# Performance work log

Measured on AMD Instinct MI355X. Metric: run time of the kernel, lower is better.

The kernel has to match this reference:

```python
import jax, jax.numpy as jnp
import numpy as np

C = 256
C8 = C // 8  # query/key channels
B, T, W, H = 4, 8, 32, 32


def setup_inputs() -> dict:
    key = jax.random.key(0)
    ks = jax.random.split(key, 8)
    s = 0.05
    return {
        "x": jax.random.normal(ks[0], (B, C, T, W, H), dtype=jnp.float32),
        "wq": jax.random.normal(ks[1], (C8, C), dtype=jnp.float32) * s,
        "bq": jax.random.normal(ks[2], (C8,), dtype=jnp.float32) * s,
        "wk": jax.random.normal(ks[3], (C8, C), dtype=jnp.float32) * s,
        "bk": jax.random.normal(ks[4], (C8,), dtype=jnp.float32) * s,
        "wv": jax.random.normal(ks[5], (C, C), dtype=jnp.float32) * s,
        "bv": jax.random.normal(ks[6], (C,), dtype=jnp.float32) * s,
        "gamma": jax.random.normal(ks[7], (1,), dtype=jnp.float32),
    }


def reference(x, wq, bq, wk, bk, wv, bv, gamma):
    b, c, t, w, h = x.shape
    n = w * h
    # Faithful to torch: x.view(-1, c, w, h) is a row-major reinterpretation
    xr = jnp.reshape(x, (-1, c, n))  # (m, C, N), m = B*T
    # 1x1 convs == per-pixel linear projections
    q = jnp.einsum("oc,mcn->mno", wq, xr) + bq            # (m, N, C8)
    k = jnp.einsum("oc,mcn->mon", wk, xr) + bk[:, None]   # (m, C8, N)
    v = jnp.einsum("oc,mcn->mon", wv, xr) + bv[:, None]   # (m, C, N)
    energy = jnp.einsum("mic,mcj->mij", q, k)             # (m, N, N), unscaled
    attention = jax.nn.softmax(energy, axis=-1)
    out = jnp.einsum("mcn,mnj->mcj", v, attention)        # V @ A (as in torch code)
    out = jnp.reshape(out, (b, c, t, w, h))
    return gamma * out + x
```

## Files before the change

kernel.cpp:

```cpp
#include <hip/hip_runtime.h>

#define MB    32
#define CCH   256
#define QCH   32
#define NPIX  1024
#define SLICE (CCH * NPIX)
#define L2E   1.44269504088896340736f
#define SHIFT 32.0f

typedef __bf16          bf16x8 __attribute__((ext_vector_type(8)));
typedef __bf16          bf16x4 __attribute__((ext_vector_type(4)));
typedef float           f32x4  __attribute__((ext_vector_type(4)));
typedef unsigned int    u32x4  __attribute__((ext_vector_type(4)));
typedef unsigned short  u16x4  __attribute__((ext_vector_type(4)));

__device__ __forceinline__ unsigned short f2bf(float f) {
    unsigned int u = __builtin_bit_cast(unsigned int, f);
    u += 0x7FFFu + ((u >> 16) & 1u);
    return (unsigned short)(u >> 16);
}
__device__ __forceinline__ u16x4 cvt4(float a, float b, float c, float d) {
    bf16x4 v = { (__bf16)a, (__bf16)b, (__bf16)c, (__bf16)d };
    return __builtin_bit_cast(u16x4, v);
}
__device__ __forceinline__ float bf2f(unsigned short u) {
    unsigned int v = (unsigned int)u << 16;
    return __builtin_bit_cast(float, v);
}
__device__ __forceinline__ bf16x8 ldfrag(const unsigned short* p) {
    u32x4 u = *(const u32x4*)p;
    return __builtin_bit_cast(bf16x8, u);
}

#define WB_OFF  0u
#define QT_OFF  262144u
#define KT_OFF  2359296u
#define V_OFF   4456448u
#define A2F_OFF 21233664u
#define PU_OFF  21364736u
#define WS_NEED 88473600u

__global__ __launch_bounds__(256) void k_prep_w(
    const float* __restrict__ wq, const float* __restrict__ wk,
    const float* __restrict__ wv, unsigned short* __restrict__ Wb)
{
    int i4 = (blockIdx.x * 256 + threadIdx.x) * 4;
    int o = i4 >> 8, c = i4 & 255;
    const float* src = (o < 32) ? wq + (size_t)o * CCH + c
                     : (o < 64) ? wk + (size_t)(o - 32) * CCH + c
                                : wv + (size_t)(o - 64) * CCH + c;
    float4 v = *(const float4*)src;
    *(u16x4*)(Wb + i4) = cvt4(v.x, v.y, v.z, v.w);
}

__global__ __launch_bounds__(256) void k_proj(
    const float* __restrict__ x, const unsigned short* __restrict__ Wb,
    const float* __restrict__ bq, const float* __restrict__ bk,
    const float* __restrict__ bv,
    unsigned short* __restrict__ Qt, unsigned short* __restrict__ Kt,
    unsigned short* __restrict__ V)
{
    __shared__ unsigned short Xs[64 * 268];

    const int t = threadIdx.x, lane = t & 63, w = t >> 6;
    const int lj = lane & 15, q = lane >> 4;
    const int n0 = blockIdx.x * 64;
    const int mi = blockIdx.y;
    const float* xp = x + (size_t)mi * SLICE;

#pragma unroll
    for (int r = 0; r < 8; ++r) {
        int job = t + r * 256;
        int cp = job >> 4;
        int seg = job & 15;
        float4 va = *(const float4*)(xp + (size_t)(2 * cp) * NPIX + n0 + seg * 4);
        float4 vb = *(const float4*)(xp + (size_t)(2 * cp + 1) * NPIX + n0 + seg * 4);
        u16x4 da = cvt4(va.x, va.y, va.z, va.w);
        u16x4 db = cvt4(vb.x, vb.y, vb.z, vb.w);
#pragma unroll
        for (int e = 0; e < 4; ++e) {
            unsigned pk = (unsigned)da[e] | ((unsigned)db[e] << 16);
            *(unsigned*)&Xs[(seg * 4 + e) * 268 + 2 * cp] = pk;
        }
    }
    __syncthreads();

    f32x4 acc[5][4];
#pragma unroll
    for (int i = 0; i < 5; ++i)
#pragma unroll
        for (int b = 0; b < 4; ++b) acc[i][b] = (f32x4){0.f, 0.f, 0.f, 0.f};

    const unsigned short* wbase = Wb + (size_t)(w * 16 + lj) * CCH + q * 8;
    const unsigned short* xbase = &Xs[lj * 268 + q * 8];

#pragma unroll 2
    for (int kc = 0; kc < CCH; kc += 32) {
        bf16x8 a[5];
#pragma unroll
        for (int i = 0; i < 5; ++i)
            a[i] = ldfrag(wbase + (size_t)i * 64 * CCH + kc);
        bf16x8 xb[4];
#pragma unroll
        for (int b = 0; b < 4; ++b)
            xb[b] = ldfrag(xbase + b * 16 * 268 + kc);
#pragma unroll
        for (int i = 0; i < 5; ++i)
#pragma unroll
            for (int b = 0; b < 4; ++b)
                acc[i][b] = __builtin_amdgcn_mfma_f32_16x16x32_bf16(a[i], xb[b], acc[i][b], 0, 0, 0);
    }

#pragma unroll
    for (int i = 0; i < 5; ++i) {
        const int o16 = (w + 4 * i) * 16;
        const int ob = o16 + 4 * q;
        if (o16 < 32) {
            unsigned short* Qp = Qt + (size_t)mi * NPIX * QCH;
            float b0 = bq[ob], b1 = bq[ob + 1], b2 = bq[ob + 2], b3 = bq[ob + 3];
#pragma unroll
            for (int b = 0; b < 4; ++b) {
                int n = n0 + b * 16 + lj;
                *(u16x4*)(Qp + (size_t)n * QCH + ob) =
                    cvt4((acc[i][b][0] + b0) * L2E, (acc[i][b][1] + b1) * L2E,
                         (acc[i][b][2] + b2) * L2E, (acc[i][b][3] + b3) * L2E);
            }
        } else if (o16 < 64) {
            unsigned short* Kp = Kt + (size_t)mi * NPIX * QCH;
            int o2 = ob - 32;
            float b0 = bk[o2], b1 = bk[o2 + 1], b2 = bk[o2 + 2], b3 = bk[o2 + 3];
#pragma unroll
            for (int b = 0; b < 4; ++b) {
                int n = n0 + b * 16 + lj;
                *(u16x4*)(Kp + (size_t)n * QCH + o2) =
                    cvt4(acc[i][b][0] + b0, acc[i][b][1] + b1,
                         acc[i][b][2] + b2, acc[i][b][3] + b3);
            }
        } else {
            unsigned short* Vw = V + (size_t)mi * SLICE;
            const int c16 = (o16 - 64) >> 4;
            const int n05 = n0 >> 5;
            const int cb = (o16 - 64) + 4 * q;
            float bb[4] = { bv[cb], bv[cb + 1], bv[cb + 2], bv[cb + 3] };
            const int ni = lj & 7;
#pragma unroll
            for (int b = 0; b < 4; ++b) {
                int n5 = n05 + (b >> 1);
                int fl = ((2 * b + (lj >> 3)) & 3) * 16 + 4 * q;
                size_t base = ((size_t)(c16 * 32 + n5) * 64 + fl) * 8 + ni;
#pragma unroll
                for (int r = 0; r < 4; ++r)
                    Vw[base + (size_t)r * 8] = f2bf(acc[i][b][r] + bb[r]);
            }
        }
    }
}

__global__ __launch_bounds__(256) void k_stats(
    const unsigned short* __restrict__ Qt, const unsigned short* __restrict__ Kt,
    float* __restrict__ a2f)
{
    const int t = threadIdx.x, lane = t & 63, w = t >> 6;
    const int lj = lane & 15, q = lane >> 4;
    const int n16 = blockIdx.x * 64 + w * 16;
    const int mi = blockIdx.y;
    const unsigned short* Qp = Qt + (size_t)mi * NPIX * QCH;
    const unsigned short* Kp = Kt + (size_t)mi * NPIX * QCH;

    bf16x8 qa = ldfrag(Qp + (size_t)(n16 + lj) * QCH + q * 8);

    float s[4] = { 0.f, 0.f, 0.f, 0.f };
#pragma unroll 8
    for (int jc = 0; jc < NPIX; jc += 16) {
        bf16x8 kb = ldfrag(Kp + (size_t)(jc + lj) * QCH + q * 8);
        f32x4 z = (f32x4){0.f, 0.f, 0.f, 0.f};
        f32x4 e = __builtin_amdgcn_mfma_f32_16x16x32_bf16(qa, kb, z, 0, 0, 0);
#pragma unroll
        for (int r = 0; r < 4; ++r) s[r] += exp2f(e[r] - SHIFT);
    }
#pragma unroll
    for (int msk = 1; msk <= 8; msk <<= 1)
#pragma unroll
        for (int r = 0; r < 4; ++r) s[r] += __shfl_xor(s[r], msk, 64);
    if (lj == 0) {
        float* apo = a2f + (size_t)mi * NPIX;
#pragma unroll
        for (int r = 0; r < 4; ++r)
            apo[n16 + 4 * q + r] = SHIFT + log2f(s[r]);
    }
}

__global__ __launch_bounds__(256) void k_pu(
    const unsigned short* __restrict__ Qt, const unsigned short* __restrict__ Kt,
    const float* __restrict__ a2f, unsigned short* __restrict__ Pu)
{
    __shared__ unsigned short Ps[4][32][36];

    const int t = threadIdx.x, lane = t & 63, w = t >> 6;
    const int lj = lane & 15, q = lane >> 4;
    const int nb = blockIdx.x >> 1;
    const int jh = blockIdx.x & 1;
    const int nw = nb * 128 + w * 32;
    const int mi = blockIdx.y;
    const unsigned short* Qp = Qt + (size_t)mi * NPIX * QCH;
    const unsigned short* Kp = Kt + (size_t)mi * NPIX * QCH;
    const float* ap = a2f + (size_t)mi * NPIX;
    unsigned short* Pup = Pu + (size_t)mi * NPIX * NPIX;

    bf16x8 qa[2];
    f32x4  a4[2];
#pragma unroll
    for (int h = 0; h < 2; ++h) {
        qa[h] = ldfrag(Qp + (size_t)(nw + h * 16 + lj) * QCH + q * 8);
        a4[h] = *(const f32x4*)(ap + nw + h * 16 + 4 * q);
    }

    const int jbeg = jh * 512;
#pragma unroll 2
    for (int jc = jbeg; jc < jbeg + 512; jc += 32) {
#pragma unroll
        for (int f = 0; f < 2; ++f) {
            bf16x8 kb = ldfrag(Kp + (size_t)(jc + f * 16 + lj) * QCH + q * 8);
#pragma unroll
            for (int h = 0; h < 2; ++h) {
                f32x4 z = (f32x4){0.f, 0.f, 0.f, 0.f};
                f32x4 e = __builtin_amdgcn_mfma_f32_16x16x32_bf16(qa[h], kb, z, 0, 0, 0);
                *(u16x4*)&Ps[w][f * 16 + lj][h * 16 + 4 * q] =
                    cvt4(exp2f(e[0] - a4[h][0]), exp2f(e[1] - a4[h][1]),
                         exp2f(e[2] - a4[h][2]), exp2f(e[3] - a4[h][3]));
            }
        }
#pragma unroll
        for (int f = 0; f < 2; ++f) {
            u32x4 bfrag = *(const u32x4*)&Ps[w][f * 16 + lj][q * 8];
            *(u32x4*)(Pup + ((size_t)((jc >> 4) + f) * 32 + (nw >> 5)) * 512 + lane * 8) = bfrag;
        }
    }
}

__global__ __launch_bounds__(256) void k_gemm_out(
    const float* __restrict__ x, const float* __restrict__ gamma,
    const unsigned short* __restrict__ Vf, const unsigned short* __restrict__ Pu,
    float* __restrict__ out)
{
    __shared__ unsigned short Vs[2][2 * 8 * 512];

    const int b = blockIdx.x;
    const int mi  = (b & 7) | ((b >> 7) << 3);
    const int sub = (b >> 3) & 15;
    const int j0  = (sub & 7) * 128;
    const int cb  = sub >> 3;

    const int t = threadIdx.x, lane = t & 63, w = t >> 6;
    const int lj = lane & 15, q = lane >> 4;
    const int jw = j0 + w * 32;

    const unsigned short* Vp  = Vf + (size_t)mi * SLICE;
    const unsigned short* Pup = Pu + (size_t)mi * NPIX * NPIX
                              + ((size_t)(jw >> 4) * 32) * 512 + lane * 8;

    const int ctl = t >> 5, ln0 = (t & 31) * 2;
    const unsigned short* vsrc0 = Vp + ((size_t)(cb * 8 + ctl) * 32) * 512 + ln0 * 8;

    f32x4 acc[8][2];
#pragma unroll
    for (int ci = 0; ci < 8; ++ci)
#pragma unroll
        for (int f = 0; f < 2; ++f) acc[ci][f] = (f32x4){0.f, 0.f, 0.f, 0.f};

    {
        u32x4 a0 = *(const u32x4*)(vsrc0);
        u32x4 a1 = *(const u32x4*)(vsrc0 + 8);
        u32x4 b0 = *(const u32x4*)(vsrc0 + 512);
        u32x4 b1 = *(const u32x4*)(vsrc0 + 520);
        *(u32x4*)&Vs[0][ctl * 512 + ln0 * 8]            = a0;
        *(u32x4*)&Vs[0][ctl * 512 + ln0 * 8 + 8]        = a1;
        *(u32x4*)&Vs[0][4096 + ctl * 512 + ln0 * 8]     = b0;
        *(u32x4*)&Vs[0][4096 + ctl * 512 + ln0 * 8 + 8] = b1;
    }
    bf16x8 pf[2][2];
#pragma unroll
    for (int h = 0; h < 2; ++h)
#pragma unroll
        for (int f = 0; f < 2; ++f)
            pf[h][f] = ldfrag(Pup + f * 16384 + (size_t)h * 512);
    __syncthreads();

    int p = 0;
    for (int nc = 0; nc < NPIX; nc += 64, p ^= 1) {
        const int nn = (nc + 64) & (NPIX - 1);
        const unsigned short* vsrc = vsrc0 + (size_t)(nn >> 5) * 512;
        u32x4 nv0 = *(const u32x4*)vsrc;
        u32x4 nv1 = *(const u32x4*)(vsrc + 8);
        u32x4 nv2 = *(const u32x4*)(vsrc + 512);
        u32x4 nv3 = *(const u32x4*)(vsrc + 520);
        bf16x8 pf_n[2][2];
#pragma unroll
        for (int h = 0; h < 2; ++h)
#pragma unroll
            for (int f = 0; f < 2; ++f)
                pf_n[h][f] = ldfrag(Pup + f * 16384 + ((size_t)(nn >> 5) + h) * 512);

        __builtin_amdgcn_s_setprio(1);
#pragma unroll
        for (int h = 0; h < 2; ++h) {
#pragma unroll
            for (int ci = 0; ci < 8; ++ci) {
                bf16x8 vfr = ldfrag(&Vs[p][h * 4096 + ci * 512 + lane * 8]);
#pragma unroll
                for (int f = 0; f < 2; ++f)
                    acc[ci][f] = __builtin_amdgcn_mfma_f32_16x16x32_bf16(vfr, pf[h][f], acc[ci][f], 0, 0, 0);
            }
        }
        __builtin_amdgcn_s_setprio(0);

        *(u32x4*)&Vs[p ^ 1][ctl * 512 + ln0 * 8]            = nv0;
        *(u32x4*)&Vs[p ^ 1][ctl * 512 + ln0 * 8 + 8]        = nv1;
        *(u32x4*)&Vs[p ^ 1][4096 + ctl * 512 + ln0 * 8]     = nv2;
        *(u32x4*)&Vs[p ^ 1][4096 + ctl * 512 + ln0 * 8 + 8] = nv3;
        __syncthreads();
#pragma unroll
        for (int h = 0; h < 2; ++h)
#pragma unroll
            for (int f = 0; f < 2; ++f) pf[h][f] = pf_n[h][f];
    }

    const float g = gamma[0];
    const size_t obase = (size_t)mi * SLICE;
#pragma unroll
    for (int ci = 0; ci < 8; ++ci) {
#pragma unroll
        for (int f = 0; f < 2; ++f) {
#pragma unroll
            for (int r = 0; r < 4; ++r) {
                int c = cb * 128 + ci * 16 + 4 * q + r;
                int j = jw + f * 16 + lj;
                size_t off = obase + (size_t)c * NPIX + j;
                out[off] = g * acc[ci][f][r] + x[off];
            }
        }
    }
}

__global__ __launch_bounds__(256) void k_attn_out(
    const float* __restrict__ x, const float* __restrict__ gamma,
    const unsigned short* __restrict__ Qt, const unsigned short* __restrict__ Kt,
    const unsigned short* __restrict__ Vf, const float* __restrict__ a2f,
    float* __restrict__ out)
{
    __shared__ unsigned short Vs[2][8 * 512];
    __shared__ unsigned short Ps[4][32][36];

    const int b = blockIdx.x;
    const int mi  = (b & 7) | ((b >> 7) << 3);
    const int sub = (b >> 3) & 15;
    const int j0  = (sub & 7) * 128;
    const int cb  = sub >> 3;

    const int t = threadIdx.x, lane = t & 63, w = t >> 6;
    const int lj = lane & 15, q = lane >> 4;
    const int jw = j0 + w * 32;

    const unsigned short* Qp = Qt + (size_t)mi * NPIX * QCH;
    const unsigned short* Kp = Kt + (size_t)mi * NPIX * QCH;
    const unsigned short* Vp = Vf + (size_t)mi * SLICE;
    const float* ap = a2f + (size_t)mi * NPIX;

    bf16x8 kb[2];
#pragma unroll
    for (int sj = 0; sj < 2; ++sj)
        kb[sj] = ldfrag(Kp + (size_t)(jw + sj * 16 + lj) * QCH + q * 8);

    const int ctl = t >> 5, ln0 = (t & 31) * 2;
    const unsigned short* vsrc0 = Vp + ((size_t)(cb * 8 + ctl) * 32) * 512 + ln0 * 8;

    f32x4 acc[8][2];
#pragma unroll
    for (int ci = 0; ci < 8; ++ci)
#pragma unroll
        for (int ji = 0; ji < 2; ++ji) acc[ci][ji] = (f32x4){0.f, 0.f, 0.f, 0.f};

    {
        u32x4 d0 = *(const u32x4*)vsrc0;
        u32x4 d1 = *(const u32x4*)(vsrc0 + 8);
        *(u32x4*)&Vs[0][ctl * 512 + ln0 * 8] = d0;
        *(u32x4*)&Vs[0][ctl * 512 + ln0 * 8 + 8] = d1;
    }
    bf16x8 qa_n[2];
    f32x4  a4_n[2];
#pragma unroll
    for (int sn = 0; sn < 2; ++sn) {
        qa_n[sn] = ldfrag(Qp + (size_t)(sn * 16 + lj) * QCH + q * 8);
        a4_n[sn] = *(const f32x4*)(ap + sn * 16 + 4 * q);
    }
    __syncthreads();

    int p = 0;
    for (int nc = 0; nc < NPIX; nc += 32, p ^= 1) {
        const int nn = (nc + 32) & (NPIX - 1);
        const unsigned short* vsrc = vsrc0 + (size_t)(nn >> 5) * 512;
        u32x4 nv0 = *(const u32x4*)vsrc;
        u32x4 nv1 = *(const u32x4*)(vsrc + 8);

        bf16x8 qa0 = qa_n[0], qa1 = qa_n[1];
        f32x4 a40 = a4_n[0], a41 = a4_n[1];
#pragma unroll
        for (int sj = 0; sj < 2; ++sj) {
            f32x4 z = (f32x4){0.f, 0.f, 0.f, 0.f};
            f32x4 e0 = __builtin_amdgcn_mfma_f32_16x16x32_bf16(qa0, kb[sj], z, 0, 0, 0);
            f32x4 e1 = __builtin_amdgcn_mfma_f32_16x16x32_bf16(qa1, kb[sj], z, 0, 0, 0);
            *(u16x4*)&Ps[w][sj * 16 + lj][4 * q] =
                cvt4(exp2f(e0[0] - a40[0]), exp2f(e0[1] - a40[1]),
                     exp2f(e0[2] - a40[2]), exp2f(e0[3] - a40[3]));
            *(u16x4*)&Ps[w][sj * 16 + lj][16 + 4 * q] =
                cvt4(exp2f(e1[0] - a41[0]), exp2f(e1[1] - a41[1]),
                     exp2f(e1[2] - a41[2]), exp2f(e1[3] - a41[3]));
        }
#pragma unroll
        for (int sn = 0; sn < 2; ++sn) {
            qa_n[sn] = ldfrag(Qp + (size_t)(nn + sn * 16 + lj) * QCH + q * 8);
            a4_n[sn] = *(const f32x4*)(ap + nn + sn * 16 + 4 * q);
        }

        bf16x8 pf[2];
#pragma unroll
        for (int ji = 0; ji < 2; ++ji)
            pf[ji] = ldfrag(&Ps[w][ji * 16 + lj][q * 8]);
#pragma unroll
        for (int ci = 0; ci < 8; ++ci) {
            bf16x8 vfr = ldfrag(&Vs[p][ci * 512 + lane * 8]);
#pragma unroll
            for (int ji = 0; ji < 2; ++ji)
                acc[ci][ji] = __builtin_amdgcn_mfma_f32_16x16x32_bf16(vfr, pf[ji], acc[ci][ji], 0, 0, 0);
        }

        *(u32x4*)&Vs[p ^ 1][ctl * 512 + ln0 * 8] = nv0;
        *(u32x4*)&Vs[p ^ 1][ctl * 512 + ln0 * 8 + 8] = nv1;
        __syncthreads();
    }

    const float g = gamma[0];
    const size_t obase = (size_t)mi * SLICE;
#pragma unroll
    for (int ci = 0; ci < 8; ++ci) {
#pragma unroll
        for (int ji = 0; ji < 2; ++ji) {
#pragma unroll
            for (int r = 0; r < 4; ++r) {
                int c = cb * 128 + ci * 16 + 4 * q + r;
                int j = jw + ji * 16 + lj;
                size_t off = obase + (size_t)c * NPIX + j;
                out[off] = g * acc[ci][ji][r] + x[off];
            }
        }
    }
}

extern "C" void kernel_launch(void* const* d_in, const int* in_sizes, int n_in,
                              void* d_out, int out_size, void* d_ws, size_t ws_size,
                              hipStream_t stream)
{
    const float* x     = (const float*)d_in[0];
    const float* wq    = (const float*)d_in[1];
    const float* bq    = (const float*)d_in[2];
    const float* wk    = (const float*)d_in[3];
    const float* bk    = (const float*)d_in[4];
    const float* wv    = (const float*)d_in[5];
    const float* bv    = (const float*)d_in[6];
    const float* gamma = (const float*)d_in[7];
    float* out = (float*)d_out;

    char* wsb = (char*)d_ws;
    unsigned short* Wb = (unsigned short*)(wsb + WB_OFF);
    unsigned short* Qt = (unsigned short*)(wsb + QT_OFF);
    unsigned short* Kt = (unsigned short*)(wsb + KT_OFF);
    unsigned short* V  = (unsigned short*)(wsb + V_OFF);
    float*          a2 = (float*)(wsb + A2F_OFF);
    unsigned short* Pu = (unsigned short*)(wsb + PU_OFF);

    k_prep_w<<<80, 256, 0, stream>>>(wq, wk, wv, Wb);
    k_proj<<<dim3(NPIX / 64, MB), 256, 0, stream>>>(x, Wb, bq, bk, bv, Qt, Kt, V);
    k_stats<<<dim3(NPIX / 64, MB), 256, 0, stream>>>(Qt, Kt, a2);

    if (ws_size >= (size_t)WS_NEED) {
        k_pu<<<dim3(16, MB), 256, 0, stream>>>(Qt, Kt, a2, Pu);
        k_gemm_out<<<512, 256, 0, stream>>>(x, gamma, V, Pu, out);
    } else {
        k_attn_out<<<512, 256, 0, stream>>>(x, gamma, Qt, Kt, V, a2, out);
    }
}
```

Before: 172.8 us.

## Split attention GEMM and P kernels finer, deepen P prefetch, vectorize V stores

In k_gemm_out each block now covers 64 channels instead of 128, so the grid doubles to 1024 blocks, and the launch bound asks for 4 blocks per CU. The P-fragment prefetch goes two stages ahead to hide global load latency. k_pu splits the j range into four chunks so it launches twice as many blocks. k_proj swaps the MFMA operands for the V rows so each lane can write V in a transposed layout with 64-bit stores instead of scalar 16-bit stores. The finer GEMM split makes each P tile be read twice as often and trades per-block reuse for occupancy.

```diff
diff --git a/kernel.cpp b/kernel.cpp
--- a/kernel.cpp
+++ b/kernel.cpp
@@ -108,49 +108,48 @@
         for (int i = 0; i < 5; ++i)
 #pragma unroll
             for (int b = 0; b < 4; ++b)
-                acc[i][b] = __builtin_amdgcn_mfma_f32_16x16x32_bf16(a[i], xb[b], acc[i][b], 0, 0, 0);
+                acc[i][b] = (i == 0)
+                    ? __builtin_amdgcn_mfma_f32_16x16x32_bf16(a[i], xb[b], acc[i][b], 0, 0, 0)
+                    : __builtin_amdgcn_mfma_f32_16x16x32_bf16(xb[b], a[i], acc[i][b], 0, 0, 0);
     }
 
 #pragma unroll
     for (int i = 0; i < 5; ++i) {
-        const int o16 = (w + 4 * i) * 16;
-        const int ob = o16 + 4 * q;
-        if (o16 < 32) {
-            unsigned short* Qp = Qt + (size_t)mi * NPIX * QCH;
-            float b0 = bq[ob], b1 = bq[ob + 1], b2 = bq[ob + 2], b3 = bq[ob + 3];
-#pragma unroll
-            for (int b = 0; b < 4; ++b) {
-                int n = n0 + b * 16 + lj;
-                *(u16x4*)(Qp + (size_t)n * QCH + ob) =
-                    cvt4((acc[i][b][0] + b0) * L2E, (acc[i][b][1] + b1) * L2E,
-                         (acc[i][b][2] + b2) * L2E, (acc[i][b][3] + b3) * L2E);
-            }
-        } else if (o16 < 64) {
-            unsigned short* Kp = Kt + (size_t)mi * NPIX * QCH;
-            int o2 = ob - 32;
-            float b0 = bk[o2], b1 = bk[o2 + 1], b2 = bk[o2 + 2], b3 = bk[o2 + 3];
-#pragma unroll
-            for (int b = 0; b < 4; ++b) {
-                int n = n0 + b * 16 + lj;
-                *(u16x4*)(Kp + (size_t)n * QCH + o2) =
-                    cvt4(acc[i][b][0] + b0, acc[i][b][1] + b1,
-                         acc[i][b][2] + b2, acc[i][b][3] + b3);
+        if (i == 0) {
+            const int ob = w * 16 + 4 * q;
+            if (w < 2) {
+                unsigned short* Qp = Qt + (size_t)mi * NPIX * QCH;
+                float b0 = bq[ob], b1 = bq[ob + 1], b2 = bq[ob + 2], b3 = bq[ob + 3];
+#pragma unroll
+                for (int b = 0; b < 4; ++b) {
+                    int n = n0 + b * 16 + lj;
+                    *(u16x4*)(Qp + (size_t)n * QCH + ob) =
+                        cvt4((acc[i][b][0] + b0) * L2E, (acc[i][b][1] + b1) * L2E,
+                             (acc[i][b][2] + b2) * L2E, (acc[i][b][3] + b3) * L2E);
+                }
+            } else {
+                unsigned short* Kp = Kt + (size_t)mi * NPIX * QCH;
+                int o2 = ob - 32;
+                float b0 = bk[o2], b1 = bk[o2 + 1], b2 = bk[o2 + 2], b3 = bk[o2 + 3];
+#pragma unroll
+                for (int b = 0; b < 4; ++b) {
+                    int n = n0 + b * 16 + lj;
+                    *(u16x4*)(Kp + (size_t)n * QCH + o2) =
+                        cvt4(acc[i][b][0] + b0, acc[i][b][1] + b1,
+                             acc[i][b][2] + b2, acc[i][b][3] + b3);
+                }
             }
         } else {
             unsigned short* Vw = V + (size_t)mi * SLICE;
-            const int c16 = (o16 - 64) >> 4;
+            const int c16 = w + 4 * (i - 1);
+            const float bb = bv[c16 * 16 + lj];
             const int n05 = n0 >> 5;
-            const int cb = (o16 - 64) + 4 * q;
-            float bb[4] = { bv[cb], bv[cb + 1], bv[cb + 2], bv[cb + 3] };
-            const int ni = lj & 7;
 #pragma unroll
             for (int b = 0; b < 4; ++b) {
-                int n5 = n05 + (b >> 1);
-                int fl = ((2 * b + (lj >> 3)) & 3) * 16 + 4 * q;
-                size_t base = ((size_t)(c16 * 32 + n5) * 64 + fl) * 8 + ni;
-#pragma unroll
-                for (int r = 0; r < 4; ++r)
-                    Vw[base + (size_t)r * 8] = f2bf(acc[i][b][r] + bb[r]);
+                const int l = lj | (((b & 1) * 2 + (q >> 1)) << 4);
+                size_t base = ((size_t)(c16 * 32 + n05 + (b >> 1)) * 64 + l) * 8 + (q & 1) * 4;
+                *(u16x4*)(Vw + base) = cvt4(acc[i][b][0] + bb, acc[i][b][1] + bb,
+                                            acc[i][b][2] + bb, acc[i][b][3] + bb);
             }
         }
     }
@@ -198,8 +197,8 @@
 
     const int t = threadIdx.x, lane = t & 63, w = t >> 6;
     const int lj = lane & 15, q = lane >> 4;
-    const int nb = blockIdx.x >> 1;
-    const int jh = blockIdx.x & 1;
+    const int nb = blockIdx.x >> 2;
+    const int jh = blockIdx.x & 3;
     const int nw = nb * 128 + w * 32;
     const int mi = blockIdx.y;
     const unsigned short* Qp = Qt + (size_t)mi * NPIX * QCH;
@@ -215,9 +214,9 @@
         a4[h] = *(const f32x4*)(ap + nw + h * 16 + 4 * q);
     }
 
-    const int jbeg = jh * 512;
+    const int jbeg = jh * 256;
 #pragma unroll 2
-    for (int jc = jbeg; jc < jbeg + 512; jc += 32) {
+    for (int jc = jbeg; jc < jbeg + 256; jc += 32) {
 #pragma unroll
         for (int f = 0; f < 2; ++f) {
             bf16x8 kb = ldfrag(Kp + (size_t)(jc + f * 16 + lj) * QCH + q * 8);
@@ -238,16 +237,16 @@
     }
 }
 
-__global__ __launch_bounds__(256) void k_gemm_out(
+__global__ __launch_bounds__(256, 4) void k_gemm_out(
     const float* __restrict__ x, const float* __restrict__ gamma,
     const unsigned short* __restrict__ Vf, const unsigned short* __restrict__ Pu,
     float* __restrict__ out)
 {
-    __shared__ unsigned short Vs[2][2 * 8 * 512];
+    __shared__ unsigned short Vs[2][4096];
 
     const int b = blockIdx.x;
-    const int mi  = (b & 7) | ((b >> 7) << 3);
-    const int sub = (b >> 3) & 15;
+    const int mi  = (b & 7) | ((b >> 8) << 3);
+    const int sub = (b >> 3) & 31;
     const int j0  = (sub & 7) * 128;
     const int cb  = sub >> 3;
 
@@ -259,54 +258,53 @@
     const unsigned short* Pup = Pu + (size_t)mi * NPIX * NPIX
                               + ((size_t)(jw >> 4) * 32) * 512 + lane * 8;
 
-    const int ctl = t >> 5, ln0 = (t & 31) * 2;
-    const unsigned short* vsrc0 = Vp + ((size_t)(cb * 8 + ctl) * 32) * 512 + ln0 * 8;
-
-    f32x4 acc[8][2];
-#pragma unroll
-    for (int ci = 0; ci < 8; ++ci)
+    const int fs = t >> 5;
+    const int ln0 = (t & 31) * 2;
+    const unsigned short* vsrc0 = Vp
+        + ((size_t)((cb * 4 + (fs & 3)) * 32) + (fs >> 2)) * 512 + ln0 * 8;
+
+    f32x4 acc[4][2];
+#pragma unroll
+    for (int ci = 0; ci < 4; ++ci)
 #pragma unroll
         for (int f = 0; f < 2; ++f) acc[ci][f] = (f32x4){0.f, 0.f, 0.f, 0.f};
 
     {
-        u32x4 a0 = *(const u32x4*)(vsrc0);
-        u32x4 a1 = *(const u32x4*)(vsrc0 + 8);
-        u32x4 b0 = *(const u32x4*)(vsrc0 + 512);
-        u32x4 b1 = *(const u32x4*)(vsrc0 + 520);
-        *(u32x4*)&Vs[0][ctl * 512 + ln0 * 8]            = a0;
-        *(u32x4*)&Vs[0][ctl * 512 + ln0 * 8 + 8]        = a1;
-        *(u32x4*)&Vs[0][4096 + ctl * 512 + ln0 * 8]     = b0;
-        *(u32x4*)&Vs[0][4096 + ctl * 512 + ln0 * 8 + 8] = b1;
-    }
-    bf16x8 pf[2][2];
+        u32x4 d0 = *(const u32x4*)vsrc0;
+        u32x4 d1 = *(const u32x4*)(vsrc0 + 8);
+        *(u32x4*)&Vs[0][fs * 512 + ln0 * 8] = d0;
+        *(u32x4*)&Vs[0][fs * 512 + ln0 * 8 + 8] = d1;
+    }
+    bf16x8 pf[2][2], pfN[2][2];
 #pragma unroll
     for (int h = 0; h < 2; ++h)
 #pragma unroll
-        for (int f = 0; f < 2; ++f)
-            pf[h][f] = ldfrag(Pup + f * 16384 + (size_t)h * 512);
+        for (int f = 0; f < 2; ++f) {
+            pf[h][f]  = ldfrag(Pup + f * 16384 + (size_t)h * 512);
+            pfN[h][f] = ldfrag(Pup + f * 16384 + (size_t)(2 + h) * 512);
+        }
     __syncthreads();
 
     int p = 0;
     for (int nc = 0; nc < NPIX; nc += 64, p ^= 1) {
-        const int nn = (nc + 64) & (NPIX - 1);
-        const unsigned short* vsrc = vsrc0 + (size_t)(nn >> 5) * 512;
-        u32x4 nv0 = *(const u32x4*)vsrc;
-        u32x4 nv1 = *(const u32x4*)(vsrc + 8);
-        u32x4 nv2 = *(const u32x4*)(vsrc + 512);
-        u32x4 nv3 = *(const u32x4*)(vsrc + 520);
-        bf16x8 pf_n[2][2];
+        const int n1 = (nc + 64) & (NPIX - 1);
+        const int n2 = (nc + 128) & (NPIX - 1);
+        const unsigned short* vs = vsrc0 + (size_t)(n1 >> 6) * 1024;
+        u32x4 nv0 = *(const u32x4*)vs;
+        u32x4 nv1 = *(const u32x4*)(vs + 8);
+        bf16x8 pf2[2][2];
 #pragma unroll
         for (int h = 0; h < 2; ++h)
 #pragma unroll
             for (int f = 0; f < 2; ++f)
-                pf_n[h][f] = ldfrag(Pup + f * 16384 + ((size_t)(nn >> 5) + h) * 512);
+                pf2[h][f] = ldfrag(Pup + f * 16384 + ((size_t)(n2 >> 5) + h) * 512);
 
         __builtin_amdgcn_s_setprio(1);
 #pragma unroll
         for (int h = 0; h < 2; ++h) {
 #pragma unroll
-            for (int ci = 0; ci < 8; ++ci) {
-                bf16x8 vfr = ldfrag(&Vs[p][h * 4096 + ci * 512 + lane * 8]);
+            for (int ci = 0; ci < 4; ++ci) {
+                bf16x8 vfr = ldfrag(&Vs[p][(h * 4 + ci) * 512 + lane * 8]);
 #pragma unroll
                 for (int f = 0; f < 2; ++f)
                     acc[ci][f] = __builtin_amdgcn_mfma_f32_16x16x32_bf16(vfr, pf[h][f], acc[ci][f], 0, 0, 0);
@@ -314,26 +312,24 @@
         }
         __builtin_amdgcn_s_setprio(0);
 
-        *(u32x4*)&Vs[p ^ 1][ctl * 512 + ln0 * 8]            = nv0;
-        *(u32x4*)&Vs[p ^ 1][ctl * 512 + ln0 * 8 + 8]        = nv1;
-        *(u32x4*)&Vs[p ^ 1][4096 + ctl * 512 + ln0 * 8]     = nv2;
-        *(u32x4*)&Vs[p ^ 1][4096 + ctl * 512 + ln0 * 8 + 8] = nv3;
+        *(u32x4*)&Vs[p ^ 1][fs * 512 + ln0 * 8] = nv0;
+        *(u32x4*)&Vs[p ^ 1][fs * 512 + ln0 * 8 + 8] = nv1;
         __syncthreads();
 #pragma unroll
         for (int h = 0; h < 2; ++h)
 #pragma unroll
-            for (int f = 0; f < 2; ++f) pf[h][f] = pf_n[h][f];
+            for (int f = 0; f < 2; ++f) { pf[h][f] = pfN[h][f]; pfN[h][f] = pf2[h][f]; }
     }
 
     const float g = gamma[0];
     const size_t obase = (size_t)mi * SLICE;
 #pragma unroll
-    for (int ci = 0; ci < 8; ++ci) {
+    for (int ci = 0; ci < 4; ++ci) {
 #pragma unroll
         for (int f = 0; f < 2; ++f) {
 #pragma unroll
             for (int r = 0; r < 4; ++r) {
-                int c = cb * 128 + ci * 16 + 4 * q + r;
+                int c = cb * 64 + ci * 16 + 4 * q + r;
                 int j = jw + f * 16 + lj;
                 size_t off = obase + (size_t)c * NPIX + j;
                 out[off] = g * acc[ci][f][r] + x[off];
@@ -483,8 +479,8 @@
     k_stats<<<dim3(NPIX / 64, MB), 256, 0, stream>>>(Qt, Kt, a2);
 
     if (ws_size >= (size_t)WS_NEED) {
-        k_pu<<<dim3(16, MB), 256, 0, stream>>>(Qt, Kt, a2, Pu);
-        k_gemm_out<<<512, 256, 0, stream>>>(x, gamma, V, Pu, out);
+        k_pu<<<dim3(32, MB), 256, 0, stream>>>(Qt, Kt, a2, Pu);
+        k_gemm_out<<<1024, 256, 0, stream>>>(x, gamma, V, Pu, out);
     } else {
         k_attn_out<<<512, 256, 0, stream>>>(x, gamma, Qt, Kt, V, a2, out);
     }
```

After: 163.1 us. 5.6% less time.
